# Kernel tuning notes

Measured on AMD Instinct MI355X. Metric: run time of the kernel, lower is better.

The kernel has to match this reference:

```python
import jax, jax.numpy as jnp
import numpy as np


def _dequant_linear(x, wq, scale):
    # wq: int [out, in], scale: [out] per-output-channel
    w = wq.astype(jnp.float32) * scale[:, None]  # dequantize
    return jnp.einsum('bsh,oh->bso', x, w)


def setup_inputs() -> dict:
    key = jax.random.key(0)
    ks = jax.random.split(key, 7)
    B, S, H, I = 2, 2048, 4096, 14336
    x = jax.random.normal(ks[0], (B, S, H), dtype=jnp.float32)
    gate_wq = jax.random.randint(ks[1], (I, H), -128, 128, dtype=jnp.int32)
    up_wq = jax.random.randint(ks[2], (I, H), -128, 128, dtype=jnp.int32)
    down_wq = jax.random.randint(ks[3], (H, I), -128, 128, dtype=jnp.int32)
    # small positive per-channel scales (~1/(127*sqrt(fan_in)))
    gate_scale = jax.random.uniform(ks[4], (I,), dtype=jnp.float32, minval=0.5, maxval=1.5) / (127.0 * np.sqrt(H))
    up_scale = jax.random.uniform(ks[5], (I,), dtype=jnp.float32, minval=0.5, maxval=1.5) / (127.0 * np.sqrt(H))
    down_scale = jax.random.uniform(ks[6], (H,), dtype=jnp.float32, minval=0.5, maxval=1.5) / (127.0 * np.sqrt(I))
    return {'x': x, 'gate_wq': gate_wq, 'gate_scale': gate_scale,
            'up_wq': up_wq, 'up_scale': up_scale,
            'down_wq': down_wq, 'down_scale': down_scale}


def reference(x, gate_wq, gate_scale, up_wq, up_scale, down_wq, down_scale):
    gate = _dequant_linear(x, gate_wq, gate_scale)   # [B,S,I]
    up = _dequant_linear(x, up_wq, up_scale)         # [B,S,I]
    h = jax.nn.silu(gate) * up                       # SwiGLU
    return _dequant_linear(h, down_wq, down_scale)   # [B,S,H]
```

## Files before the change

kernel.cpp:

```cpp
#include <hip/hip_runtime.h>

typedef __bf16 bf16x8 __attribute__((ext_vector_type(8)));
typedef float f32x4 __attribute__((ext_vector_type(4)));

__device__ __forceinline__ unsigned short f2bf(float f) {
  unsigned u = __float_as_uint(f);
  u += 0x7FFFu + ((u >> 16) & 1u);
  return (unsigned short)(u >> 16);
}

__device__ __forceinline__ void async16(const void* g, void* l) {
  __builtin_amdgcn_global_load_lds((const __attribute__((address_space(1))) void*)g,
                                   (__attribute__((address_space(3))) void*)l,
                                   16, 0, 0);
}

__global__ void cvt_f32_bf16_k(const float4* __restrict__ in, ushort4* __restrict__ out) {
  int i = blockIdx.x * blockDim.x + threadIdx.x;
  float4 v = in[i];
  ushort4 o;
  o.x = f2bf(v.x); o.y = f2bf(v.y); o.z = f2bf(v.z); o.w = f2bf(v.w);
  out[i] = o;
}

__global__ void cvt_i32_bf16_k(const int4* __restrict__ in, ushort4* __restrict__ out) {
  int i = blockIdx.x * blockDim.x + threadIdx.x;
  int4 v = in[i];
  ushort4 o;
  o.x = f2bf((float)v.x); o.y = f2bf((float)v.y);
  o.z = f2bf((float)v.z); o.w = f2bf((float)v.w);
  out[i] = o;
}

#define BAR() do { asm volatile("" ::: "memory"); __builtin_amdgcn_s_barrier(); \
                   asm volatile("" ::: "memory"); } while (0)

#define STAGE2(GP, LP) do { async16((GP), (LP)); \
    async16((GP) + 8 * (size_t)K, (LP) + 8 * 64); } while (0)

#define LOAD_A(AF, CURA, HA)                                                   \
  _Pragma("unroll") for (int mi = 0; mi < 4; ++mi)                             \
  _Pragma("unroll") for (int kk = 0; kk < 2; ++kk)                             \
    AF[mi][kk] = *(const bf16x8*)&(CURA)[((HA) * 128 + wrow + mi * 16 + r) * 64 \
                                         + (((kk * 4 + q) ^ rx) * 8)];

#define LOAD_B(BF, CURB, HB)                                                   \
  _Pragma("unroll") for (int ni = 0; ni < 2; ++ni)                             \
  _Pragma("unroll") for (int kk = 0; kk < 2; ++kk)                             \
    BF[ni][kk] = *(const bf16x8*)&(CURB)[((HB) * 128 + wcol + ni * 16 + r) * 64 \
                                         + (((kk * 4 + q) ^ rx) * 8)];

#define MFMA16(ACC, AF, BF)                                                    \
  __builtin_amdgcn_s_setprio(1);                                               \
  _Pragma("unroll") for (int kk = 0; kk < 2; ++kk)                             \
  _Pragma("unroll") for (int ni = 0; ni < 2; ++ni)                             \
  _Pragma("unroll") for (int mi = 0; mi < 4; ++mi)                             \
    ACC[mi][ni] = __builtin_amdgcn_mfma_f32_16x16x32_bf16(                     \
        AF[mi][kk], BF[ni][kk], ACC[mi][ni], 0, 0, 0);                         \
  __builtin_amdgcn_s_setprio(0);

__global__ __launch_bounds__(512, 2)
void gemm_gateup(const unsigned short* __restrict__ A,
                 const unsigned short* __restrict__ Bg,
                 const unsigned short* __restrict__ Bu,
                 const float* __restrict__ gsc, const float* __restrict__ usc,
                 unsigned short* __restrict__ Hout,
                 int M, int N, int K) {
  __shared__ unsigned short sA [2 * 256 * 64];
  __shared__ unsigned short sBg[2 * 128 * 64];
  __shared__ unsigned short sBu[2 * 128 * 64];

  const int tid  = threadIdx.x;
  const int lane = tid & 63;
  const int wv   = tid >> 6;

  const int bid = blockIdx.x;
  const int grp = bid >> 8;
  const int rem = bid & 255;
  const int bN  = ((grp << 4) + (rem & 15)) * 128;
  const int bM  = (rem >> 4) * 256;

  const int srow = lane >> 3;
  const int gcol = ((lane & 7) ^ srow) * 8;

  const unsigned short* gA0 = A  + (size_t)(bM +       wv * 16 + srow) * K + gcol;
  const unsigned short* gA1 = A  + (size_t)(bM + 128 + wv * 16 + srow) * K + gcol;
  const unsigned short* gBg = Bg + (size_t)(bN +       wv * 16 + srow) * K + gcol;
  const unsigned short* gBu = Bu + (size_t)(bN +       wv * 16 + srow) * K + gcol;

  const int r    = lane & 15;
  const int q    = lane >> 4;
  const int rx   = r & 7;
  const int wrow = (wv >> 2) * 64;
  const int wcol = (wv & 3) * 32;

  f32x4 accg0[4][2], accg1[4][2], accu0[4][2], accu1[4][2];
#pragma unroll
  for (int i = 0; i < 4; i++)
#pragma unroll
    for (int j = 0; j < 2; j++) {
      accg0[i][j] = f32x4{0.f, 0.f, 0.f, 0.f};
      accg1[i][j] = f32x4{0.f, 0.f, 0.f, 0.f};
      accu0[i][j] = f32x4{0.f, 0.f, 0.f, 0.f};
      accu1[i][j] = f32x4{0.f, 0.f, 0.f, 0.f};
    }

  const int NT = K >> 6;

  STAGE2(gA0, &sA [ wv * 16 * 64]);
  STAGE2(gBg, &sBg[ wv * 16 * 64]);
  STAGE2(gBu, &sBu[ wv * 16 * 64]);
  STAGE2(gA1, &sA [(128 + wv * 16) * 64]);
  asm volatile("s_waitcnt vmcnt(4)" ::: "memory");
  __builtin_amdgcn_s_barrier();

  int cur = 0;
  for (int t = 0; t < NT; ++t) {
    const unsigned short* curA  = sA  + cur * (256 * 64);
    const unsigned short* curBg = sBg + cur * (128 * 64);
    const unsigned short* curBu = sBu + cur * (128 * 64);
    unsigned short* nxtA  = sA  + (cur ^ 1) * (256 * 64);
    unsigned short* nxtBg = sBg + (cur ^ 1) * (128 * 64);
    unsigned short* nxtBu = sBu + (cur ^ 1) * (128 * 64);
    const int  kn = (t + 1) << 6;
    const bool st = (t + 1) < NT;

    bf16x8 af0[4][2], af1[4][2];

    {
      bf16x8 bfr[2][2];
      LOAD_A(af0, curA, 0);
      LOAD_B(bfr, curBg, 0);
      if (st) STAGE2(gA0 + kn, nxtA + wv * 16 * 64);
      BAR();
      MFMA16(accg0, af0, bfr);
      if (st) asm volatile("s_waitcnt vmcnt(4)" ::: "memory");
      else    asm volatile("s_waitcnt vmcnt(2)" ::: "memory");
      BAR();
    }
    {
      bf16x8 bfr[2][2];
      LOAD_B(bfr, curBu, 0);
      if (st) STAGE2(gBg + kn, nxtBg + wv * 16 * 64);
      BAR();
      MFMA16(accu0, af0, bfr);
      if (st) asm volatile("s_waitcnt vmcnt(4)" ::: "memory");
      else    asm volatile("s_waitcnt vmcnt(0)" ::: "memory");
      BAR();
    }
    {
      bf16x8 bfr[2][2];
      LOAD_A(af1, curA, 1);
      LOAD_B(bfr, curBg, 0);
      if (st) STAGE2(gBu + kn, nxtBu + wv * 16 * 64);
      BAR();
      MFMA16(accg1, af1, bfr);
      BAR();
    }
    {
      bf16x8 bfr[2][2];
      LOAD_B(bfr, curBu, 0);
      if (st) STAGE2(gA1 + kn, nxtA + (128 + wv * 16) * 64);
      BAR();
      MFMA16(accu1, af1, bfr);
      if (st) {
        asm volatile("s_waitcnt vmcnt(4)" ::: "memory");
        BAR();
      }
    }
    cur ^= 1;
  }

#pragma unroll
  for (int ni = 0; ni < 2; ++ni) {
    const int col = bN + wcol + ni * 16 + r;
    const float gs = gsc[col], us = usc[col];
#pragma unroll
    for (int mi = 0; mi < 4; ++mi) {
#pragma unroll
      for (int rr = 0; rr < 4; ++rr) {
        const int row0 = bM + wrow + mi * 16 + q * 4 + rr;
        float g0 = accg0[mi][ni][rr] * gs;
        float u0 = accu0[mi][ni][rr] * us;
        Hout[(size_t)row0 * N + col] = f2bf((g0 / (1.f + __expf(-g0))) * u0);
        const int row1 = row0 + 128;
        float g1 = accg1[mi][ni][rr] * gs;
        float u1 = accu1[mi][ni][rr] * us;
        Hout[(size_t)row1 * N + col] = f2bf((g1 / (1.f + __expf(-g1))) * u1);
      }
    }
  }
}

__global__ __launch_bounds__(512, 2)
void gemm_down(const unsigned short* __restrict__ A,
               const unsigned short* __restrict__ B,
               const float* __restrict__ dsc,
               float* __restrict__ out,
               int M, int N, int K) {
  __shared__ unsigned short sA[2 * 256 * 64];
  __shared__ unsigned short sB[2 * 256 * 64];

  const int tid  = threadIdx.x;
  const int lane = tid & 63;
  const int wv   = tid >> 6;

  const int bM = (blockIdx.x >> 4) * 256;
  const int bN = (blockIdx.x & 15) * 256;

  const int srow = lane >> 3;
  const int gcol = ((lane & 7) ^ srow) * 8;

  const unsigned short* gA0 = A + (size_t)(bM +       wv * 16 + srow) * K + gcol;
  const unsigned short* gA1 = A + (size_t)(bM + 128 + wv * 16 + srow) * K + gcol;
  const unsigned short* gB0 = B + (size_t)(bN +       wv * 16 + srow) * K + gcol;
  const unsigned short* gB1 = B + (size_t)(bN + 128 + wv * 16 + srow) * K + gcol;

  const int r    = lane & 15;
  const int q    = lane >> 4;
  const int rx   = r & 7;
  const int wrow = (wv >> 2) * 64;
  const int wcol = (wv & 3) * 32;

  f32x4 a00[4][2], a01[4][2], a10[4][2], a11[4][2];
#pragma unroll
  for (int i = 0; i < 4; i++)
#pragma unroll
    for (int j = 0; j < 2; j++) {
      a00[i][j] = f32x4{0.f, 0.f, 0.f, 0.f};
      a01[i][j] = f32x4{0.f, 0.f, 0.f, 0.f};
      a10[i][j] = f32x4{0.f, 0.f, 0.f, 0.f};
      a11[i][j] = f32x4{0.f, 0.f, 0.f, 0.f};
    }

  const int NT = K >> 6;

  STAGE2(gA0, &sA[ wv * 16 * 64]);
  STAGE2(gB0, &sB[ wv * 16 * 64]);
  STAGE2(gB1, &sB[(128 + wv * 16) * 64]);
  STAGE2(gA1, &sA[(128 + wv * 16) * 64]);
  asm volatile("s_waitcnt vmcnt(4)" ::: "memory");
  __builtin_amdgcn_s_barrier();

  int cur = 0;
  for (int t = 0; t < NT; ++t) {
    const unsigned short* curA = sA + cur * (256 * 64);
    const unsigned short* curB = sB + cur * (256 * 64);
    unsigned short* nxtA = sA + (cur ^ 1) * (256 * 64);
    unsigned short* nxtB = sB + (cur ^ 1) * (256 * 64);
    const int  kn = (t + 1) << 6;
    const bool st = (t + 1) < NT;

    bf16x8 af0[4][2], af1[4][2];

    {
      bf16x8 bfr[2][2];
      LOAD_A(af0, curA, 0);
      LOAD_B(bfr, curB, 0);
      if (st) STAGE2(gA0 + kn, nxtA + wv * 16 * 64);
      BAR();
      MFMA16(a00, af0, bfr);
      if (st) asm volatile("s_waitcnt vmcnt(4)" ::: "memory");
      else    asm volatile("s_waitcnt vmcnt(2)" ::: "memory");
      BAR();
    }
    {
      bf16x8 bfr[2][2];
      LOAD_B(bfr, curB, 1);
      if (st) STAGE2(gB0 + kn, nxtB + wv * 16 * 64);
      BAR();
      MFMA16(a01, af0, bfr);
      if (st) asm volatile("s_waitcnt vmcnt(4)" ::: "memory");
      else    asm volatile("s_waitcnt vmcnt(0)" ::: "memory");
      BAR();
    }
    {
      bf16x8 bfr[2][2];
      LOAD_A(af1, curA, 1);
      LOAD_B(bfr, curB, 0);
      if (st) STAGE2(gB1 + kn, nxtB + (128 + wv * 16) * 64);
      BAR();
      MFMA16(a10, af1, bfr);
      BAR();
    }
    {
      bf16x8 bfr[2][2];
      LOAD_B(bfr, curB, 1);
      if (st) STAGE2(gA1 + kn, nxtA + (128 + wv * 16) * 64);
      BAR();
      MFMA16(a11, af1, bfr);
      if (st) {
        asm volatile("s_waitcnt vmcnt(4)" ::: "memory");
        BAR();
      }
    }
    cur ^= 1;
  }

#pragma unroll
  for (int ni = 0; ni < 2; ++ni) {
    const int c0 = bN + wcol + ni * 16 + r;
    const int c1 = c0 + 128;
    const float s0 = dsc[c0], s1 = dsc[c1];
#pragma unroll
    for (int mi = 0; mi < 4; ++mi) {
#pragma unroll
      for (int rr = 0; rr < 4; ++rr) {
        const int row0 = bM + wrow + mi * 16 + q * 4 + rr;
        const int row1 = row0 + 128;
        out[(size_t)row0 * N + c0] = a00[mi][ni][rr] * s0;
        out[(size_t)row0 * N + c1] = a01[mi][ni][rr] * s1;
        out[(size_t)row1 * N + c0] = a10[mi][ni][rr] * s0;
        out[(size_t)row1 * N + c1] = a11[mi][ni][rr] * s1;
      }
    }
  }
}

extern "C" void kernel_launch(void* const* d_in, const int* in_sizes, int n_in,
                              void* d_out, int out_size, void* d_ws, size_t ws_size,
                              hipStream_t stream) {
  constexpr int M  = 4096;
  constexpr int Hd = 4096;
  constexpr int Id = 14336;

  const float* x   = (const float*)d_in[0];
  const int*   gwq = (const int*)  d_in[1];
  const float* gsc = (const float*)d_in[2];
  const int*   uwq = (const int*)  d_in[3];
  const float* usc = (const float*)d_in[4];
  const int*   dwq = (const int*)  d_in[5];
  const float* dsc = (const float*)d_in[6];
  float* out = (float*)d_out;

  unsigned short* xb = (unsigned short*)d_ws;
  unsigned short* w0 = xb + (size_t)M * Hd;
  unsigned short* wu = w0 + (size_t)Id * Hd;
  unsigned short* hb = wu + (size_t)Id * Hd;

  cvt_f32_bf16_k<<<(M * Hd) / 1024, 256, 0, stream>>>((const float4*)x, (ushort4*)xb);
  cvt_i32_bf16_k<<<((size_t)Id * Hd) / 1024, 256, 0, stream>>>((const int4*)gwq, (ushort4*)w0);
  cvt_i32_bf16_k<<<((size_t)Id * Hd) / 1024, 256, 0, stream>>>((const int4*)uwq, (ushort4*)wu);

  gemm_gateup<<<(M / 256) * (Id / 128), 512, 0, stream>>>(xb, w0, wu, gsc, usc, hb, M, Id, Hd);

  cvt_i32_bf16_k<<<((size_t)Hd * Id) / 1024, 256, 0, stream>>>((const int4*)dwq, (ushort4*)w0);

  gemm_down<<<(M / 256) * (Hd / 256), 512, 0, stream>>>(hb, w0, dsc, out, M, Hd, Id);
}
```

Baseline: 2.179 ms.

## Replace pipelined gate/up GEMM with simpler 128x128 tile kernel; remap down-GEMM blocks

The gate/up GEMM's double-buffered 512-thread kernel with a 256x128 tile is replaced by a single-buffered 256-thread kernel on 128x128 tiles. Each wave computes a 64x64 sub-tile for both gate and up, and the grid doubles in block count. The down GEMM gets a block-index remap, an XCD-aware swizzle of the M/N tile order. Dropping double buffering loses load/compute overlap and lowers reuse per tile, while the simpler code may improve occupancy and L2 locality.

```diff
diff --git a/kernel.cpp b/kernel.cpp
--- a/kernel.cpp
+++ b/kernel.cpp
@@ -30,6 +30,109 @@
   o.x = f2bf((float)v.x); o.y = f2bf((float)v.y);
   o.z = f2bf((float)v.z); o.w = f2bf((float)v.w);
   out[i] = o;
+}
+
+__global__ __launch_bounds__(256, 2)
+void gemm_gateup(const unsigned short* __restrict__ A,
+                 const unsigned short* __restrict__ Bg,
+                 const unsigned short* __restrict__ Bu,
+                 const float* __restrict__ gsc, const float* __restrict__ usc,
+                 unsigned short* __restrict__ Hout,
+                 int M, int N, int K) {
+  __shared__ unsigned short sA[128 * 64];
+  __shared__ unsigned short sBg[128 * 64];
+  __shared__ unsigned short sBu[128 * 64];
+
+  const int tid  = threadIdx.x;
+  const int lane = tid & 63;
+  const int wv   = tid >> 6;
+
+  const int bid = blockIdx.x;
+  const int grp = bid >> 8;
+  const int rem = bid & 255;
+  const int bN  = ((grp << 3) + (rem & 7)) * 128;
+  const int bM  = (rem >> 3) * 128;
+
+  const int srow = lane >> 3;
+  const int gcol = ((lane & 7) ^ srow) * 8;
+
+  const unsigned short* gA  = A  + (size_t)(bM + wv * 32 + srow) * K + gcol;
+  const unsigned short* gBg = Bg + (size_t)(bN + wv * 32 + srow) * K + gcol;
+  const unsigned short* gBu = Bu + (size_t)(bN + wv * 32 + srow) * K + gcol;
+  unsigned short* lA  = &sA [(wv * 32) * 64];
+  unsigned short* lBg = &sBg[(wv * 32) * 64];
+  unsigned short* lBu = &sBu[(wv * 32) * 64];
+
+  const int r  = lane & 15;
+  const int q  = lane >> 4;
+  const int rx = r & 7;
+  const int wm = (wv >> 1) * 64;
+  const int wn = (wv & 1) * 64;
+
+  f32x4 accg[4][4], accu[4][4];
+#pragma unroll
+  for (int i = 0; i < 4; i++)
+#pragma unroll
+    for (int j = 0; j < 4; j++) {
+      accg[i][j] = f32x4{0.f, 0.f, 0.f, 0.f};
+      accu[i][j] = f32x4{0.f, 0.f, 0.f, 0.f};
+    }
+
+  for (int k0 = 0; k0 < K; k0 += 64) {
+    const unsigned short* pA = gA + k0;
+    async16(pA,                  lA);
+    async16(pA +  8 * (size_t)K, lA +  8 * 64);
+    async16(pA + 16 * (size_t)K, lA + 16 * 64);
+    async16(pA + 24 * (size_t)K, lA + 24 * 64);
+    const unsigned short* pG = gBg + k0;
+    async16(pG,                  lBg);
+    async16(pG +  8 * (size_t)K, lBg +  8 * 64);
+    async16(pG + 16 * (size_t)K, lBg + 16 * 64);
+    async16(pG + 24 * (size_t)K, lBg + 24 * 64);
+    const unsigned short* pU = gBu + k0;
+    async16(pU,                  lBu);
+    async16(pU +  8 * (size_t)K, lBu +  8 * 64);
+    async16(pU + 16 * (size_t)K, lBu + 16 * 64);
+    async16(pU + 24 * (size_t)K, lBu + 24 * 64);
+    __syncthreads();
+
+#pragma unroll
+    for (int kk = 0; kk < 2; ++kk) {
+      const int pc = ((kk * 4 + q) ^ rx) * 8;
+      bf16x8 af[4];
+#pragma unroll
+      for (int mi = 0; mi < 4; mi++)
+        af[mi] = *(const bf16x8*)&sA[(wm + mi * 16 + r) * 64 + pc];
+#pragma unroll
+      for (int ni = 0; ni < 4; ni++) {
+        bf16x8 bg = *(const bf16x8*)&sBg[(wn + ni * 16 + r) * 64 + pc];
+        bf16x8 bu = *(const bf16x8*)&sBu[(wn + ni * 16 + r) * 64 + pc];
+#pragma unroll
+        for (int mi = 0; mi < 4; mi++) {
+          accg[mi][ni] = __builtin_amdgcn_mfma_f32_16x16x32_bf16(af[mi], bg, accg[mi][ni], 0, 0, 0);
+          accu[mi][ni] = __builtin_amdgcn_mfma_f32_16x16x32_bf16(af[mi], bu, accu[mi][ni], 0, 0, 0);
+        }
+      }
+    }
+    __syncthreads();
+  }
+
+#pragma unroll
+  for (int ni = 0; ni < 4; ni++) {
+    const int col = bN + wn + ni * 16 + r;
+    const float gs = gsc[col], us = usc[col];
+#pragma unroll
+    for (int mi = 0; mi < 4; mi++) {
+#pragma unroll
+      for (int rr = 0; rr < 4; rr++) {
+        const int row = bM + wm + mi * 16 + q * 4 + rr;
+        float g = accg[mi][ni][rr] * gs;
+        float u = accu[mi][ni][rr] * us;
+        float hv = (g / (1.f + __expf(-g))) * u;
+        Hout[(size_t)row * N + col] = f2bf(hv);
+      }
+    }
+  }
 }
 
 #define BAR() do { asm volatile("" ::: "memory"); __builtin_amdgcn_s_barrier(); \
@@ -60,139 +163,6 @@
   __builtin_amdgcn_s_setprio(0);
 
 __global__ __launch_bounds__(512, 2)
-void gemm_gateup(const unsigned short* __restrict__ A,
-                 const unsigned short* __restrict__ Bg,
-                 const unsigned short* __restrict__ Bu,
-                 const float* __restrict__ gsc, const float* __restrict__ usc,
-                 unsigned short* __restrict__ Hout,
-                 int M, int N, int K) {
-  __shared__ unsigned short sA [2 * 256 * 64];
-  __shared__ unsigned short sBg[2 * 128 * 64];
-  __shared__ unsigned short sBu[2 * 128 * 64];
-
-  const int tid  = threadIdx.x;
-  const int lane = tid & 63;
-  const int wv   = tid >> 6;
-
-  const int bid = blockIdx.x;
-  const int grp = bid >> 8;
-  const int rem = bid & 255;
-  const int bN  = ((grp << 4) + (rem & 15)) * 128;
-  const int bM  = (rem >> 4) * 256;
-
-  const int srow = lane >> 3;
-  const int gcol = ((lane & 7) ^ srow) * 8;
-
-  const unsigned short* gA0 = A  + (size_t)(bM +       wv * 16 + srow) * K + gcol;
-  const unsigned short* gA1 = A  + (size_t)(bM + 128 + wv * 16 + srow) * K + gcol;
-  const unsigned short* gBg = Bg + (size_t)(bN +       wv * 16 + srow) * K + gcol;
-  const unsigned short* gBu = Bu + (size_t)(bN +       wv * 16 + srow) * K + gcol;
-
-  const int r    = lane & 15;
-  const int q    = lane >> 4;
-  const int rx   = r & 7;
-  const int wrow = (wv >> 2) * 64;
-  const int wcol = (wv & 3) * 32;
-
-  f32x4 accg0[4][2], accg1[4][2], accu0[4][2], accu1[4][2];
-#pragma unroll
-  for (int i = 0; i < 4; i++)
-#pragma unroll
-    for (int j = 0; j < 2; j++) {
-      accg0[i][j] = f32x4{0.f, 0.f, 0.f, 0.f};
-      accg1[i][j] = f32x4{0.f, 0.f, 0.f, 0.f};
-      accu0[i][j] = f32x4{0.f, 0.f, 0.f, 0.f};
-      accu1[i][j] = f32x4{0.f, 0.f, 0.f, 0.f};
-    }
-
-  const int NT = K >> 6;
-
-  STAGE2(gA0, &sA [ wv * 16 * 64]);
-  STAGE2(gBg, &sBg[ wv * 16 * 64]);
-  STAGE2(gBu, &sBu[ wv * 16 * 64]);
-  STAGE2(gA1, &sA [(128 + wv * 16) * 64]);
-  asm volatile("s_waitcnt vmcnt(4)" ::: "memory");
-  __builtin_amdgcn_s_barrier();
-
-  int cur = 0;
-  for (int t = 0; t < NT; ++t) {
-    const unsigned short* curA  = sA  + cur * (256 * 64);
-    const unsigned short* curBg = sBg + cur * (128 * 64);
-    const unsigned short* curBu = sBu + cur * (128 * 64);
-    unsigned short* nxtA  = sA  + (cur ^ 1) * (256 * 64);
-    unsigned short* nxtBg = sBg + (cur ^ 1) * (128 * 64);
-    unsigned short* nxtBu = sBu + (cur ^ 1) * (128 * 64);
-    const int  kn = (t + 1) << 6;
-    const bool st = (t + 1) < NT;
-
-    bf16x8 af0[4][2], af1[4][2];
-
-    {
-      bf16x8 bfr[2][2];
-      LOAD_A(af0, curA, 0);
-      LOAD_B(bfr, curBg, 0);
-      if (st) STAGE2(gA0 + kn, nxtA + wv * 16 * 64);
-      BAR();
-      MFMA16(accg0, af0, bfr);
-      if (st) asm volatile("s_waitcnt vmcnt(4)" ::: "memory");
-      else    asm volatile("s_waitcnt vmcnt(2)" ::: "memory");
-      BAR();
-    }
-    {
-      bf16x8 bfr[2][2];
-      LOAD_B(bfr, curBu, 0);
-      if (st) STAGE2(gBg + kn, nxtBg + wv * 16 * 64);
-      BAR();
-      MFMA16(accu0, af0, bfr);
-      if (st) asm volatile("s_waitcnt vmcnt(4)" ::: "memory");
-      else    asm volatile("s_waitcnt vmcnt(0)" ::: "memory");
-      BAR();
-    }
-    {
-      bf16x8 bfr[2][2];
-      LOAD_A(af1, curA, 1);
-      LOAD_B(bfr, curBg, 0);
-      if (st) STAGE2(gBu + kn, nxtBu + wv * 16 * 64);
-      BAR();
-      MFMA16(accg1, af1, bfr);
-      BAR();
-    }
-    {
-      bf16x8 bfr[2][2];
-      LOAD_B(bfr, curBu, 0);
-      if (st) STAGE2(gA1 + kn, nxtA + (128 + wv * 16) * 64);
-      BAR();
-      MFMA16(accu1, af1, bfr);
-      if (st) {
-        asm volatile("s_waitcnt vmcnt(4)" ::: "memory");
-        BAR();
-      }
-    }
-    cur ^= 1;
-  }
-
-#pragma unroll
-  for (int ni = 0; ni < 2; ++ni) {
-    const int col = bN + wcol + ni * 16 + r;
-    const float gs = gsc[col], us = usc[col];
-#pragma unroll
-    for (int mi = 0; mi < 4; ++mi) {
-#pragma unroll
-      for (int rr = 0; rr < 4; ++rr) {
-        const int row0 = bM + wrow + mi * 16 + q * 4 + rr;
-        float g0 = accg0[mi][ni][rr] * gs;
-        float u0 = accu0[mi][ni][rr] * us;
-        Hout[(size_t)row0 * N + col] = f2bf((g0 / (1.f + __expf(-g0))) * u0);
-        const int row1 = row0 + 128;
-        float g1 = accg1[mi][ni][rr] * gs;
-        float u1 = accu1[mi][ni][rr] * us;
-        Hout[(size_t)row1 * N + col] = f2bf((g1 / (1.f + __expf(-g1))) * u1);
-      }
-    }
-  }
-}
-
-__global__ __launch_bounds__(512, 2)
 void gemm_down(const unsigned short* __restrict__ A,
                const unsigned short* __restrict__ B,
                const float* __restrict__ dsc,
@@ -205,8 +175,10 @@
   const int lane = tid & 63;
   const int wv   = tid >> 6;
 
-  const int bM = (blockIdx.x >> 4) * 256;
-  const int bN = (blockIdx.x & 15) * 256;
+  const int bid  = blockIdx.x;
+  const int wgid = (bid & 7) * 32 + (bid >> 3);
+  const int bM = (wgid >> 4) * 256;
+  const int bN = (wgid & 15) * 256;
 
   const int srow = lane >> 3;
   const int gcol = ((lane & 7) ^ srow) * 8;
@@ -342,7 +314,7 @@
   cvt_i32_bf16_k<<<((size_t)Id * Hd) / 1024, 256, 0, stream>>>((const int4*)gwq, (ushort4*)w0);
   cvt_i32_bf16_k<<<((size_t)Id * Hd) / 1024, 256, 0, stream>>>((const int4*)uwq, (ushort4*)wu);
 
-  gemm_gateup<<<(M / 256) * (Id / 128), 512, 0, stream>>>(xb, w0, wu, gsc, usc, hb, M, Id, Hd);
+  gemm_gateup<<<(Id / 128) * (M / 128), 256, 0, stream>>>(xb, w0, wu, gsc, usc, hb, M, Id, Hd);
 
   cvt_i32_bf16_k<<<((size_t)Hd * Id) / 1024, 256, 0, stream>>>((const int4*)dwq, (ushort4*)w0);
 
```

Measured after the change: 2.063 ms. -5.3%, faster.
